# Performance work log

Measured on AMD Instinct MI355X. Metric: run time of the kernel, lower is better.

Reference implementation:

```python
import jax, jax.numpy as jnp
import numpy as np

B, T, C, H = 2, 2048, 2048, 16
HS = C // H
AL = 10  # aligner_generator_length


def apply_rope(x, rope):
    # x: [B,T,H,HS], rope: [T, HS//2, 2] holding (cos, sin)
    xs = x.reshape(x.shape[0], x.shape[1], x.shape[2], HS // 2, 2)
    rc = rope[None, :, None]  # [1,T,1,HS//2,2]
    out = jnp.stack([
        xs[..., 0] * rc[..., 0] - xs[..., 1] * rc[..., 1],
        xs[..., 1] * rc[..., 0] + xs[..., 0] * rc[..., 1],
    ], axis=-1)
    return out.reshape(x.shape)


def setup_inputs() -> dict:
    key = jax.random.key(0)
    ks = jax.random.split(key, 5)
    x = jax.random.normal(ks[0], (B, T, C), jnp.float32)
    # real RoPE cache (cos, sin) as in lit-llama build_rope_cache
    inv_freq = 1.0 / (10000.0 ** (np.arange(0, HS, 2, dtype=np.float32) / HS))
    freqs = np.outer(np.arange(T, dtype=np.float32), inv_freq)  # [T, HS//2]
    rope = jnp.asarray(np.stack([np.cos(freqs), np.sin(freqs)], axis=-1), jnp.float32)
    mask = jnp.tril(jnp.ones((T, T), dtype=bool))[None, None]  # causal, True = attend
    W_attn = jax.random.normal(ks[1], (3 * C, C), jnp.float32) * 0.02
    W_proj = jax.random.normal(ks[2], (C, C), jnp.float32) * 0.02
    adapter_emb = jax.random.normal(ks[3], (AL, C), jnp.float32) * 0.02
    gating = jax.random.normal(ks[4], (1, H, 1, 1), jnp.float32) * 0.1
    return dict(x=x, rope=rope, mask=mask, W_attn=W_attn, W_proj=W_proj,
                adapter_emb=adapter_emb, gating=gating, max_seq_length=T)


def reference(x, rope, mask, W_attn, W_proj, adapter_emb, gating, max_seq_length):
    b, t, c = x.shape
    qkv = x @ W_attn.T  # [B,T,3C]
    q, k, v = jnp.split(qkv, 3, axis=-1)
    q = apply_rope(q.reshape(b, t, H, HS), rope).transpose(0, 2, 1, 3)  # [B,H,T,HS]
    k = apply_rope(k.reshape(b, t, H, HS), rope).transpose(0, 2, 1, 3)
    v = v.reshape(b, t, H, HS).transpose(0, 2, 1, 3)
    scale = 1.0 / jnp.sqrt(jnp.asarray(HS, x.dtype))
    # causal SDPA
    s = jnp.einsum('bhqd,bhkd->bhqk', q, k) * scale
    s = jnp.where(mask[..., :t, :t], s, jnp.asarray(-jnp.inf, s.dtype))
    y = jnp.einsum('bhqk,bhkd->bhqd', jax.nn.softmax(s, axis=-1), v)
    # adapter prefix cross-attention (aligner_generator mode)
    pqkv = adapter_emb @ W_attn.T  # [AL,3C]
    _, ak, av = jnp.split(pqkv, 3, axis=-1)
    ak = ak.reshape(AL, H, HS).transpose(1, 0, 2)[None]  # [1,H,AL,HS]
    av = av.reshape(AL, H, HS).transpose(1, 0, 2)[None]
    sa = jnp.einsum('bhqd,bhkd->bhqk', q, ak) * scale  # no mask (amask all True)
    ay = jnp.einsum('bhqk,bhkd->bhqd', jax.nn.softmax(sa, axis=-1), av)
    y = y + gating * ay
    y = y.transpose(0, 2, 1, 3).reshape(b, t, c)
    return y @ W_proj.T
```

## Files before the change

kernel.cpp:

```cpp
#include <hip/hip_runtime.h>

typedef unsigned short u16;
typedef unsigned int u32;
typedef __bf16 bf16x8 __attribute__((ext_vector_type(8)));
typedef float f32x4 __attribute__((ext_vector_type(4)));

#define B_ 2
#define T_ 2048
#define C_ 2048
#define H_ 16
#define HS_ 128
#define AL_ 10
#define C3_ 6144
#define MASKV (-3.0e38f)
#define MFMA16(a, b, c) __builtin_amdgcn_mfma_f32_16x16x32_bf16(a, b, c, 0, 0, 0)

#define GLDS16(g, l) __builtin_amdgcn_global_load_lds(                         \
    (const __attribute__((address_space(1))) u32*)(const void*)(g),            \
    (__attribute__((address_space(3))) u32*)(void*)(l), 16, 0, 0)

__device__ __forceinline__ float b2f(u16 v) {
  union { u32 u; float f; } x; x.u = ((u32)v) << 16; return x.f;
}
__device__ __forceinline__ u16 f2b(float f) {
  u32 u = __builtin_bit_cast(u32, f);
  return (u16)((u + 0x7FFFu + ((u >> 16) & 1u)) >> 16);
}
__device__ __forceinline__ float rb(float f) { return b2f(f2b(f)); }

__global__ __launch_bounds__(256) void convert_all(
    const float* __restrict__ x,  u16* __restrict__ xb,
    const float* __restrict__ Wa, u16* __restrict__ Wab,
    const float* __restrict__ Wp, u16* __restrict__ Wpb)
{
  int i = blockIdx.x * 256 + threadIdx.x;
  const float* in; u16* out;
  if (i < 1048576)      { in = x;  out = xb;  }
  else if (i < 2621440) { in = Wa; out = Wab; i -= 1048576; }
  else                  { in = Wp; out = Wpb; i -= 2621440; }
  union { float4 v[2]; float s[8]; } f;
  f.v[0] = *(const float4*)(in + (size_t)i * 8);
  f.v[1] = *(const float4*)(in + (size_t)i * 8 + 4);
  union { uint4 v; u16 e[8]; } o;
#pragma unroll
  for (int j = 0; j < 8; j++) o.e[j] = f2b(f.s[j]);
  *(uint4*)(out + (size_t)i * 8) = o.v;
}

template <bool OUTF32>
__global__ __launch_bounds__(256) void gemm_lds(
    const u16* __restrict__ Ap, const u16* __restrict__ Bp,
    void* __restrict__ Cp, int N, int K, int lda)
{
  __shared__ u16 lA[128 * 32];
  __shared__ u16 lB[128 * 32];
  const int tid  = threadIdx.x;
  const int lane = tid & 63, wave = tid >> 6;
  const int quad = lane >> 4, l16 = lane & 15;
  const int nwg = gridDim.x * gridDim.y;
  int bid = blockIdx.y * gridDim.x + blockIdx.x;
  bid = (bid & 7) * (nwg >> 3) + (bid >> 3);
  const int bm = (bid / gridDim.x) * 128, bn = (bid % gridDim.x) * 128;
  const int wm = (wave >> 1) * 64, wn = (wave & 1) * 64;

  const int r0 = wave * 16 + (lane >> 2);
  const int c0 = (lane & 3) * 8;
  const u16* ga0 = Ap + (size_t)(bm + r0) * lda + c0;
  const u16* ga1 = ga0 + (size_t)64 * lda;
  const u16* gb0 = Bp + (size_t)(bn + r0) * K + c0;
  const u16* gb1 = gb0 + (size_t)64 * K;
  u16* la0 = &lA[wave * 512];
  u16* lb0 = &lB[wave * 512];

  f32x4 acc[4][4] = {};
  for (int k0 = 0; k0 < K; k0 += 32) {
    __syncthreads();
    GLDS16(ga0, la0);
    GLDS16(ga1, la0 + 2048);
    GLDS16(gb0, lb0);
    GLDS16(gb1, lb0 + 2048);
    ga0 += 32; ga1 += 32; gb0 += 32; gb1 += 32;
    __syncthreads();
    bf16x8 af[4], bfv[4];
#pragma unroll
    for (int i = 0; i < 4; i++)
      af[i] = *(const bf16x8*)&lA[(wm + i * 16 + l16) * 32 + quad * 8];
#pragma unroll
    for (int i = 0; i < 4; i++)
      bfv[i] = *(const bf16x8*)&lB[(wn + i * 16 + l16) * 32 + quad * 8];
#pragma unroll
    for (int i = 0; i < 4; i++)
#pragma unroll
      for (int j = 0; j < 4; j++)
        acc[i][j] = MFMA16(af[i], bfv[j], acc[i][j]);
  }
#pragma unroll
  for (int i = 0; i < 4; i++) {
#pragma unroll
    for (int r = 0; r < 4; r++) {
      const int row = bm + wm + i * 16 + quad * 4 + r;
      if constexpr (OUTF32) {
        float* crow = (float*)Cp + (size_t)row * N + bn + wn + l16;
#pragma unroll
        for (int j = 0; j < 4; j++)
          crow[j * 16] = acc[i][j][r];
      } else {
        u16* crow = (u16*)Cp + (size_t)row * N + bn + wn + l16;
#pragma unroll
        for (int j = 0; j < 4; j++)
          crow[j * 16] = f2b(acc[i][j][r]);
      }
    }
  }
}

template <bool AF32, bool BF32, bool OUTF32>
__global__ __launch_bounds__(256) void gemm_nt(
    const void* __restrict__ Ap, const void* __restrict__ Bp,
    void* __restrict__ Cp, int N, int K, int lda)
{
  __shared__ u16 lA[128 * 32];
  __shared__ u16 lB[128 * 32];
  const int tid  = threadIdx.x;
  const int lane = tid & 63, wave = tid >> 6;
  const int quad = lane >> 4, l16 = lane & 15;
  const int bm = blockIdx.y * 128, bn = blockIdx.x * 128;
  const int wm = (wave >> 1) * 64, wn = (wave & 1) * 64;
  const int srow = tid >> 1, scol = (tid & 1) * 16;
  f32x4 acc[4][4] = {};

  for (int k0 = 0; k0 < K; k0 += 32) {
    __align__(16) u16 abuf[16], bbuf[16];
    if constexpr (AF32) {
      const float* gA = (const float*)Ap + (size_t)(bm + srow) * lda + scol + k0;
      union { float4 v[4]; float s[16]; } fa;
#pragma unroll
      for (int j = 0; j < 4; j++) fa.v[j] = *(const float4*)(gA + j * 4);
#pragma unroll
      for (int j = 0; j < 16; j++) abuf[j] = f2b(fa.s[j]);
    } else {
      const u16* gA = (const u16*)Ap + (size_t)(bm + srow) * lda + scol + k0;
      *(uint4*)&abuf[0] = *(const uint4*)(gA);
      *(uint4*)&abuf[8] = *(const uint4*)(gA + 8);
    }
    if constexpr (BF32) {
      const float* gB = (const float*)Bp + (size_t)(bn + srow) * K + scol + k0;
      union { float4 v[4]; float s[16]; } fb;
#pragma unroll
      for (int j = 0; j < 4; j++) fb.v[j] = *(const float4*)(gB + j * 4);
#pragma unroll
      for (int j = 0; j < 16; j++) bbuf[j] = f2b(fb.s[j]);
    } else {
      const u16* gB = (const u16*)Bp + (size_t)(bn + srow) * K + scol + k0;
      *(uint4*)&bbuf[0] = *(const uint4*)(gB);
      *(uint4*)&bbuf[8] = *(const uint4*)(gB + 8);
    }
    __syncthreads();
    *(uint4*)&lA[srow * 32 + scol]     = *(uint4*)&abuf[0];
    *(uint4*)&lA[srow * 32 + scol + 8] = *(uint4*)&abuf[8];
    *(uint4*)&lB[srow * 32 + scol]     = *(uint4*)&bbuf[0];
    *(uint4*)&lB[srow * 32 + scol + 8] = *(uint4*)&bbuf[8];
    __syncthreads();
    bf16x8 af[4], bfv[4];
#pragma unroll
    for (int i = 0; i < 4; i++)
      af[i] = *(const bf16x8*)&lA[(wm + i * 16 + l16) * 32 + quad * 8];
#pragma unroll
    for (int i = 0; i < 4; i++)
      bfv[i] = *(const bf16x8*)&lB[(wn + i * 16 + l16) * 32 + quad * 8];
#pragma unroll
    for (int i = 0; i < 4; i++)
#pragma unroll
      for (int j = 0; j < 4; j++)
        acc[i][j] = MFMA16(af[i], bfv[j], acc[i][j]);
  }
#pragma unroll
  for (int i = 0; i < 4; i++) {
#pragma unroll
    for (int r = 0; r < 4; r++) {
      const int row = bm + wm + i * 16 + quad * 4 + r;
      if constexpr (OUTF32) {
        float* crow = (float*)Cp + (size_t)row * N + bn + wn + l16;
#pragma unroll
        for (int j = 0; j < 4; j++)
          crow[j * 16] = acc[i][j][r];
      } else {
        u16* crow = (u16*)Cp + (size_t)row * N + bn + wn + l16;
#pragma unroll
        for (int j = 0; j < 4; j++)
          crow[j * 16] = f2b(acc[i][j][r]);
      }
    }
  }
}

__global__ __launch_bounds__(256) void adapter_pqkv(
    const float* __restrict__ emb, const float* __restrict__ W,
    float* __restrict__ akb, float* __restrict__ avb)
{
  const int tid = threadIdx.x;
  const int lane = tid & 63;
  const int w = blockIdx.x * 4 + (tid >> 6);
  const int part = w >> 11;
  const int col = w & 2047;
  const float* wrow = W + (size_t)(C_ + part * C_ + col) * C_;
  float acc[AL_];
#pragma unroll
  for (int l = 0; l < AL_; l++) acc[l] = 0.f;
  for (int i = 0; i < 32; i++) {
    const int c = i * 64 + lane;
    const float wv = rb(wrow[c]);
#pragma unroll
    for (int l = 0; l < AL_; l++) acc[l] += wv * rb(emb[l * C_ + c]);
  }
#pragma unroll
  for (int l = 0; l < AL_; l++) {
    for (int off = 32; off > 0; off >>= 1) acc[l] += __shfl_xor(acc[l], off);
  }
  if (lane == 0) {
    const int h = col >> 7, d = col & 127;
    float* dst = (part == 0 ? akb : avb) + (size_t)h * AL_ * HS_ + d;
#pragma unroll
    for (int l = 0; l < AL_; l++) dst[l * HS_] = acc[l];
  }
}

__global__ __launch_bounds__(256) void rope_tv(
    u16* __restrict__ qkv, const float* __restrict__ rope,
    u16* __restrict__ vt)
{
  __shared__ __align__(16) char lT[64 * 256];
  const int bid = blockIdx.x;
  if (bid < 16384) {
    const int g = bid * 256 + threadIdx.x;
    const int j2 = g & 63;
    const int h  = (g >> 6) & 15;
    const int t  = (g >> 10) & 2047;
    const int b  = g >> 21;
    u16* src = qkv + (size_t)(b * T_ + t) * C3_ + h * HS_ + j2 * 2;
    const u32 qp = *(const u32*)(src);
    const u32 kp = *(const u32*)(src + C_);
    const float2 rp = *(const float2*)(rope + (t * 64 + j2) * 2);
    const float c = rb(rp.x), s = rb(rp.y);
    const float q0 = b2f((u16)qp), q1 = b2f((u16)(qp >> 16));
    const float k0 = b2f((u16)kp), k1 = b2f((u16)(kp >> 16));
    const float qr0 = q0 * c - q1 * s, qr1 = q1 * c + q0 * s;
    const float kr0 = k0 * c - k1 * s, kr1 = k1 * c + k0 * s;
    *(u32*)(src)      = (u32)f2b(qr0) | ((u32)f2b(qr1) << 16);
    *(u32*)(src + C_) = (u32)f2b(kr0) | ((u32)f2b(kr1) << 16);
    return;
  }
  const int r = bid - 16384;
  const int tid = threadIdx.x;
  const int t0 = (r & 31) * 64, h = (r >> 5) & 15, b = r >> 9;
  const u16* Vg = qkv + (size_t)(b * T_ + t0) * C3_ + 2 * C_ + h * HS_;
#pragma unroll
  for (int i = 0; i < 4; i++) {
    const int e = (i * 256 + tid) * 8;
    const int t = e >> 7, c = e & 127;
    *(uint4*)(lT + t * 256 + ((c * 2) ^ ((t & 7) << 4))) =
        *(const uint4*)(Vg + (size_t)t * C3_ + c);
  }
  __syncthreads();
  const int d = tid >> 1, half = tid & 1;
  __align__(16) u16 out[32];
#pragma unroll
  for (int tt = 0; tt < 32; tt++) {
    const int t = half * 32 + tt;
    out[tt] = *(const u16*)(lT + t * 256 + ((d * 2) ^ ((t & 7) << 4)));
  }
  u16* dst = vt + ((size_t)(b * H_ + h) * HS_ + d) * T_ + t0 + half * 32;
  *(uint4*)(dst)      = *(const uint4*)&out[0];
  *(uint4*)(dst + 8)  = *(const uint4*)&out[8];
  *(uint4*)(dst + 16) = *(const uint4*)&out[16];
  *(uint4*)(dst + 24) = *(const uint4*)&out[24];
}

__global__ __launch_bounds__(256, 4) void attn_flash(
    u16* __restrict__ qkv, const u16* __restrict__ vt,
    const float* __restrict__ akbuf, const float* __restrict__ avbuf,
    const float* __restrict__ gating)
{
  __shared__ __align__(16) char smem[37888];
  char* smKb = smem;
  char* smVb = smem + 16384;
  char* smP  = smem + 32768;

  const int tid  = threadIdx.x;
  const int lane = tid & 63, wave = tid >> 6;
  const int quad = lane >> 4, l16 = lane & 15;
  const int bx = blockIdx.x, h = blockIdx.y, b = blockIdx.z;
  const u16* Kg = qkv + (size_t)(b * T_) * C3_ + C_ + h * HS_;
  const u16* Vt = vt + (size_t)(b * H_ + h) * HS_ * T_;
  const float scale = 0.08838834764831845f;

  const int krow = wave * 4 + (lane >> 4);
  const int kco  = (((lane & 15) * 16) ^ ((krow & 7) << 4)) >> 1;
  const int vd0 = wave * 16 + (lane >> 2);
  const int vco = (((lane & 3) * 16) ^ (((vd0 >> 1) & 3) << 4)) >> 1;
  const int vsw = ((l16 >> 1) & 3) << 4;

#define STAGE_KV(KT, BUF) do {                                                 \
    char* kb_ = smKb + (BUF) * 8192 + wave * 1024;                             \
    char* vb_ = smVb + (BUF) * 8192 + wave * 1024;                             \
    const u16* ks0_ = Kg + (size_t)((KT) * 32 + krow) * C3_ + kco;             \
    const u16* ks1_ = Kg + (size_t)((KT) * 32 + 16 + krow) * C3_ + kco;        \
    GLDS16(ks0_, kb_);                                                         \
    GLDS16(ks1_, kb_ + 4096);                                                  \
    const u16* vs0_ = Vt + (size_t)vd0 * T_ + (KT) * 32 + vco;                 \
    const u16* vs1_ = Vt + (size_t)(vd0 + 64) * T_ + (KT) * 32 + vco;          \
    GLDS16(vs0_, vb_);                                                         \
    GLDS16(vs1_, vb_ + 4096);                                                  \
  } while (0)

  for (int half = 0; half < 2; half++) {
    const int qt = half ? bx : 31 - bx;
    u16* Qg = qkv + ((size_t)(b * T_) + qt * 64) * C3_ + h * HS_;

    bf16x8 qf[4];
    {
      const u16* qrow = Qg + (size_t)(wave * 16 + l16) * C3_;
#pragma unroll
      for (int kk = 0; kk < 4; kk++)
        qf[kk] = *(const bf16x8*)(qrow + kk * 32 + quad * 8);
    }

    f32x4 acc[8] = {};
    float mrun = MASKV, lrun = 0.f;
    const int nkt = (qt + 1) * 2;
    const int qg = qt * 64 + wave * 16 + l16;

    STAGE_KV(0, 0);
    __syncthreads();

    int cur = 0;
    for (int kt = 0; kt < nkt; kt++) {
      if (kt + 1 < nkt) STAGE_KV(kt + 1, cur ^ 1);
      const char* smK = smKb + cur * 8192;
      const char* smV = smVb + cur * 8192;
      f32x4 sacc[2] = {};
      const int sw = (l16 & 7) << 4;
#pragma unroll
      for (int kk = 0; kk < 4; kk++) {
        const int co = (kk * 64 + quad * 16) ^ sw;
        bf16x8 bk0 = *(const bf16x8*)(smK + l16 * 256 + co);
        bf16x8 bk1 = *(const bf16x8*)(smK + (16 + l16) * 256 + co);
        sacc[0] = MFMA16(bk0, qf[kk], sacc[0]);
        sacc[1] = MFMA16(bk1, qf[kk], sacc[1]);
      }
      float s[8];
#pragma unroll
      for (int n = 0; n < 2; n++)
#pragma unroll
        for (int r = 0; r < 4; r++) {
          float v = sacc[n][r] * scale;
          if (kt * 32 + n * 16 + quad * 4 + r > qg) v = MASKV;
          s[n * 4 + r] = v;
        }
      float rmax = fmaxf(fmaxf(fmaxf(s[0], s[1]), fmaxf(s[2], s[3])),
                         fmaxf(fmaxf(s[4], s[5]), fmaxf(s[6], s[7])));
      rmax = fmaxf(rmax, __shfl_xor(rmax, 16));
      rmax = fmaxf(rmax, __shfl_xor(rmax, 32));
      const float mnew = fmaxf(mrun, rmax);
      const float alpha = __expf(mrun - mnew);
      mrun = mnew;
      float p[8];
#pragma unroll
      for (int i = 0; i < 8; i++) p[i] = __expf(s[i] - mnew);
      float rs = ((p[0] + p[1]) + (p[2] + p[3])) + ((p[4] + p[5]) + (p[6] + p[7]));
      rs += __shfl_xor(rs, 16);
      rs += __shfl_xor(rs, 32);
      lrun = lrun * alpha + rs;
      float alr[4];
#pragma unroll
      for (int r = 0; r < 4; r++) alr[r] = __shfl(alpha, quad * 4 + r);
      {
        char* prow = smP + (wave * 16 + l16) * 80;
#pragma unroll
        for (int n = 0; n < 2; n++)
#pragma unroll
          for (int rp = 0; rp < 2; rp++) {
            const u32 w = (u32)f2b(p[n * 4 + rp * 2]) |
                          ((u32)f2b(p[n * 4 + rp * 2 + 1]) << 16);
            *(u32*)(prow + (n * 16 + quad * 4 + rp * 2) * 2) = w;
          }
      }
#pragma unroll
      for (int nt = 0; nt < 8; nt++)
#pragma unroll
        for (int r = 0; r < 4; r++) acc[nt][r] *= alr[r];
      {
        bf16x8 ap = *(const bf16x8*)(smP + (wave * 16 + l16) * 80 + quad * 16);
#pragma unroll
        for (int nt = 0; nt < 8; nt++) {
          bf16x8 bv = *(const bf16x8*)(smV + (nt * 16 + l16) * 64 +
                                       ((quad * 16) ^ vsw));
          acc[nt] = MFMA16(ap, bv, acc[nt]);
        }
      }
      __syncthreads();
      cur ^= 1;
    }
    float lr[4];
#pragma unroll
    for (int r = 0; r < 4; r++) lr[r] = __shfl(lrun, quad * 4 + r);
    float* lAk = (float*)smVb;
    float* lAv = lAk + AL_ * HS_;
    {
      const float* aks = akbuf + (size_t)h * AL_ * HS_;
      const float* avs = avbuf + (size_t)h * AL_ * HS_;
      for (int i = tid; i < AL_ * HS_; i += 256) { lAk[i] = aks[i]; lAv[i] = avs[i]; }
    }
    __syncthreads();
    const int ar = tid >> 2, ah = tid & 3;
    const u16* qr = Qg + (size_t)ar * C3_ + ah * 32;
    float sa[AL_];
#pragma unroll
    for (int l = 0; l < AL_; l++) sa[l] = 0.f;
#pragma unroll
    for (int c = 0; c < 4; c++) {
      union { uint4 v; u16 e[8]; } qv;
      qv.v = *(const uint4*)(qr + c * 8);
#pragma unroll
      for (int j = 0; j < 8; j++) {
        const float qf2 = b2f(qv.e[j]);
#pragma unroll
        for (int l = 0; l < AL_; l++)
          sa[l] += qf2 * lAk[l * HS_ + ah * 32 + c * 8 + j];
      }
    }
#pragma unroll
    for (int l = 0; l < AL_; l++) {
      sa[l] += __shfl_xor(sa[l], 1);
      sa[l] += __shfl_xor(sa[l], 2);
      sa[l] *= scale;
    }
    float smax = sa[0];
#pragma unroll
    for (int l = 1; l < AL_; l++) smax = fmaxf(smax, sa[l]);
    float ssum = 0.f;
#pragma unroll
    for (int l = 0; l < AL_; l++) { sa[l] = __expf(sa[l] - smax); ssum += sa[l]; }
    const float inv = 1.f / ssum;
#pragma unroll
    for (int l = 0; l < AL_; l++) sa[l] *= inv;
    __syncthreads();
    u16* lAy = (u16*)smem;
#pragma unroll
    for (int c = 0; c < 4; c++) {
      const int col = ah * 32 + c * 8;
      union { uint4 v; u16 e[8]; } ov;
#pragma unroll
      for (int j = 0; j < 8; j++) {
        float a = 0.f;
#pragma unroll
        for (int l = 0; l < AL_; l++) a += sa[l] * lAv[l * HS_ + col + j];
        ov.e[j] = f2b(a);
      }
      *(uint4*)(lAy + ar * HS_ + col) = ov.v;
    }
    __syncthreads();
    const float g = rb(gating[h]);
#pragma unroll
    for (int r = 0; r < 4; r++) {
      const int row = wave * 16 + quad * 4 + r;
      const float linv = 1.f / lr[r];
      u16* yrow = Qg + (size_t)row * C3_ + l16;
#pragma unroll
      for (int nt = 0; nt < 8; nt++) {
        const float v = acc[nt][r] * linv + g * b2f(lAy[row * HS_ + nt * 16 + l16]);
        yrow[nt * 16] = f2b(v);
      }
    }
    __syncthreads();
  }
#undef STAGE_KV
}

extern "C" void kernel_launch(void* const* d_in, const int* in_sizes, int n_in,
                              void* d_out, int out_size, void* d_ws, size_t ws_size,
                              hipStream_t stream) {
  (void)out_size;
  int ix = 0, irope = 1, iW = 3, iP = 4, iE = 5, iG = 6;
  for (int i = 0; i < n_in; i++) {
    switch (in_sizes[i]) {
      case 8388608:  ix = i;    break;
      case 262144:   irope = i; break;
      case 12582912: iW = i;    break;
      case 20480:    iE = i;    break;
      case 16:       iG = i;    break;
      case 4194304:  iP = i;    break;
      default: break;
    }
  }
  const float* x      = (const float*)d_in[ix];
  const float* rope   = (const float*)d_in[irope];
  const float* W_attn = (const float*)d_in[iW];
  const float* W_proj = (const float*)d_in[iP];
  const float* emb    = (const float*)d_in[iE];
  const float* gating = (const float*)d_in[iG];

  u16*   qkv = (u16*)d_ws;
  float* akb = (float*)d_out;
  float* avb = akb + (size_t)H_ * AL_ * HS_;
  u16*   vtb = (u16*)(avb + (size_t)H_ * AL_ * HS_);

  const bool fast = ws_size >= (size_t)100663296;
  if (fast) {
    u16* xb  = qkv + (size_t)25165824;
    u16* Wab = xb  + (size_t)8388608;
    u16* Wpb = Wab + (size_t)12582912;
    convert_all<<<dim3(12288), 256, 0, stream>>>(x, xb, W_attn, Wab, W_proj, Wpb);
    gemm_lds<false><<<dim3(48, 32), 256, 0, stream>>>(xb, Wab, qkv, 6144, 2048, 2048);
    adapter_pqkv<<<dim3(1024), 256, 0, stream>>>(emb, W_attn, akb, avb);
    rope_tv<<<dim3(17408), 256, 0, stream>>>(qkv, rope, vtb);
    attn_flash<<<dim3(16, 16, 2), 256, 0, stream>>>(qkv, vtb, akb, avb, gating);
    gemm_lds<true><<<dim3(16, 32), 256, 0, stream>>>(qkv, Wpb, (float*)d_out, 2048, 2048, 6144);
  } else {
    gemm_nt<true, true, false><<<dim3(48, 32), 256, 0, stream>>>(
        x, W_attn, qkv, 6144, 2048, 2048);
    adapter_pqkv<<<dim3(1024), 256, 0, stream>>>(emb, W_attn, akb, avb);
    rope_tv<<<dim3(17408), 256, 0, stream>>>(qkv, rope, vtb);
    attn_flash<<<dim3(16, 16, 2), 256, 0, stream>>>(qkv, vtb, akb, avb, gating);
    gemm_nt<false, true, true><<<dim3(16, 32), 256, 0, stream>>>(
        qkv, W_proj, (float*)d_out, 2048, 2048, 6144);
  }
}
```

Before: 512.9 us.

## Add 256x256-tile double-buffered GEMM for QKV projection

Adds a new GEMM kernel that uses 256x256 output tiles with 512 threads, a 64-wide K step, XOR-swizzled LDS layout and double-buffered global-to-LDS direct loads. The loads for the next K tile are interleaved between MFMA phases, and s_setprio is raised around the MFMA bursts. The QKV projection now uses this kernel instead of the 128x128 one. The aim is more data reuse per tile and overlap of loads with compute. The cost is only 384 workgroups at one block per CU and a 128 KB LDS footprint.

```diff
diff --git a/kernel.cpp b/kernel.cpp
--- a/kernel.cpp
+++ b/kernel.cpp
@@ -45,6 +45,145 @@
 #pragma unroll
   for (int j = 0; j < 8; j++) o.e[j] = f2b(f.s[j]);
   *(uint4*)(out + (size_t)i * 8) = o.v;
+}
+
+template <bool OUTF32>
+__global__ __launch_bounds__(512, 1) void gemm256(
+    const u16* __restrict__ Ap, const u16* __restrict__ Bp,
+    void* __restrict__ Cp, int N, int K, int lda)
+{
+  __shared__ __align__(16) u16 lds[65536];
+  const int tid  = threadIdx.x;
+  const int lane = tid & 63, wid = tid >> 6;
+  const int quad = lane >> 4, l16 = lane & 15;
+  const int wm2 = wid >> 2, wn4 = wid & 3;
+  const int nwg = gridDim.x * gridDim.y;
+  int bid = blockIdx.y * gridDim.x + blockIdx.x;
+  bid = (bid & 7) * (nwg >> 3) + (bid >> 3);
+  const int bm = (bid / gridDim.x) * 256, bn = (bid % gridDim.x) * 256;
+
+  const int srow = tid >> 3, schunk = tid & 7;
+  const int gchunk = schunk ^ (srow & 7);
+  const u16* gA = Ap + (size_t)(bm + srow) * lda + gchunk * 8;
+  const u16* gB = Bp + (size_t)(bn + srow) * K + gchunk * 8;
+
+#define ST256(T, SL, PART) do {                                                \
+    u16* d_ = lds + (SL) * 32768 + (((PART) >= 2) ? 16384 : 0)                 \
+              + ((PART) & 1) * 8192 + wid * 512;                               \
+    const size_t str_ = ((PART) >= 2) ? (size_t)K : (size_t)lda;               \
+    const u16* g_ = (((PART) >= 2) ? gB : gA) + (size_t)(T) * 64               \
+              + (size_t)((PART) & 1) * 128 * str_;                             \
+    GLDS16(g_, d_);                                                            \
+    GLDS16(g_ + 64 * str_, d_ + 4096);                                         \
+  } while (0)
+
+  f32x4 acc[8][4] = {};
+  const int nt = K >> 6;
+  const int asw = (l16 & 7) << 4;
+
+  ST256(0, 0, 0); ST256(0, 0, 1); ST256(0, 0, 2); ST256(0, 0, 3);
+  asm volatile("s_waitcnt vmcnt(0)" ::: "memory");
+  __builtin_amdgcn_s_barrier();
+  __builtin_amdgcn_sched_barrier(0);
+
+  int cur = 0;
+  for (int t = 0; t < nt; ++t) {
+    const char* sA = (const char*)(lds + cur * 32768);
+    const char* sB = sA + 32768;
+    const bool pf = (t + 1 < nt);
+    const int ns = cur ^ 1;
+    bf16x8 a[4][2], bq0[2][2], bq1[2][2];
+#pragma unroll
+    for (int m = 0; m < 4; m++)
+#pragma unroll
+      for (int kk = 0; kk < 2; kk++)
+        a[m][kk] = *(const bf16x8*)(sA + (wm2 * 128 + m * 16 + l16) * 128 +
+                                    (((kk * 4 + quad) * 16) ^ asw));
+#pragma unroll
+    for (int n = 0; n < 2; n++)
+#pragma unroll
+      for (int kk = 0; kk < 2; kk++)
+        bq0[n][kk] = *(const bf16x8*)(sB + (wn4 * 64 + n * 16 + l16) * 128 +
+                                      (((kk * 4 + quad) * 16) ^ asw));
+    if (pf) ST256(t + 1, ns, 0);
+    __builtin_amdgcn_s_setprio(1);
+#pragma unroll
+    for (int m = 0; m < 4; m++)
+#pragma unroll
+      for (int n = 0; n < 2; n++)
+#pragma unroll
+        for (int kk = 0; kk < 2; kk++)
+          acc[m][n] = MFMA16(a[m][kk], bq0[n][kk], acc[m][n]);
+    __builtin_amdgcn_s_setprio(0);
+    __builtin_amdgcn_sched_barrier(0);
+#pragma unroll
+    for (int n = 0; n < 2; n++)
+#pragma unroll
+      for (int kk = 0; kk < 2; kk++)
+        bq1[n][kk] = *(const bf16x8*)(sB + (wn4 * 64 + (n + 2) * 16 + l16) * 128 +
+                                      (((kk * 4 + quad) * 16) ^ asw));
+    if (pf) ST256(t + 1, ns, 1);
+    __builtin_amdgcn_s_setprio(1);
+#pragma unroll
+    for (int m = 0; m < 4; m++)
+#pragma unroll
+      for (int n = 0; n < 2; n++)
+#pragma unroll
+        for (int kk = 0; kk < 2; kk++)
+          acc[m][n + 2] = MFMA16(a[m][kk], bq1[n][kk], acc[m][n + 2]);
+    __builtin_amdgcn_s_setprio(0);
+    __builtin_amdgcn_sched_barrier(0);
+#pragma unroll
+    for (int m = 0; m < 4; m++)
+#pragma unroll
+      for (int kk = 0; kk < 2; kk++)
+        a[m][kk] = *(const bf16x8*)(sA + (wm2 * 128 + (m + 4) * 16 + l16) * 128 +
+                                    (((kk * 4 + quad) * 16) ^ asw));
+    if (pf) ST256(t + 1, ns, 2);
+    __builtin_amdgcn_s_setprio(1);
+#pragma unroll
+    for (int m = 0; m < 4; m++)
+#pragma unroll
+      for (int n = 0; n < 2; n++)
+#pragma unroll
+        for (int kk = 0; kk < 2; kk++)
+          acc[m + 4][n + 2] = MFMA16(a[m][kk], bq1[n][kk], acc[m + 4][n + 2]);
+    __builtin_amdgcn_s_setprio(0);
+    __builtin_amdgcn_sched_barrier(0);
+    if (pf) ST256(t + 1, ns, 3);
+    __builtin_amdgcn_s_setprio(1);
+#pragma unroll
+    for (int m = 0; m < 4; m++)
+#pragma unroll
+      for (int n = 0; n < 2; n++)
+#pragma unroll
+        for (int kk = 0; kk < 2; kk++)
+          acc[m + 4][n] = MFMA16(a[m][kk], bq0[n][kk], acc[m + 4][n]);
+    __builtin_amdgcn_s_setprio(0);
+    asm volatile("s_waitcnt vmcnt(0)" ::: "memory");
+    __builtin_amdgcn_s_barrier();
+    __builtin_amdgcn_sched_barrier(0);
+    cur ^= 1;
+  }
+#undef ST256
+#pragma unroll
+  for (int m = 0; m < 8; m++) {
+#pragma unroll
+    for (int r = 0; r < 4; r++) {
+      const int row = bm + wm2 * 128 + m * 16 + quad * 4 + r;
+      if constexpr (OUTF32) {
+        float* crow = (float*)Cp + (size_t)row * N + bn + wn4 * 64 + l16;
+#pragma unroll
+        for (int n = 0; n < 4; n++)
+          crow[n * 16] = acc[m][n][r];
+      } else {
+        u16* crow = (u16*)Cp + (size_t)row * N + bn + wn4 * 64 + l16;
+#pragma unroll
+        for (int n = 0; n < 4; n++)
+          crow[n * 16] = f2b(acc[m][n][r]);
+      }
+    }
+  }
 }
 
 template <bool OUTF32>
@@ -511,7 +650,7 @@
     u16* Wab = xb  + (size_t)8388608;
     u16* Wpb = Wab + (size_t)12582912;
     convert_all<<<dim3(12288), 256, 0, stream>>>(x, xb, W_attn, Wab, W_proj, Wpb);
-    gemm_lds<false><<<dim3(48, 32), 256, 0, stream>>>(xb, Wab, qkv, 6144, 2048, 2048);
+    gemm256<false><<<dim3(24, 16), 512, 0, stream>>>(xb, Wab, qkv, 6144, 2048, 2048);
     adapter_pqkv<<<dim3(1024), 256, 0, stream>>>(emb, W_attn, akb, avb);
     rope_tv<<<dim3(17408), 256, 0, stream>>>(qkv, rope, vtb);
     attn_flash<<<dim3(16, 16, 2), 256, 0, stream>>>(qkv, vtb, akb, avb, gating);
```

Result: faster. 486.3 us (-5.2%).
